# Kernel tuning notes

Hardware: AMD Instinct MI355X
Metric: run time of the kernel (lower is better)

The kernel has to match this reference:

```python
import jax, jax.numpy as jnp
import numpy as np

DIM_IN_Q = 4096
DIM_IN_K = 4096
MSG_DIM = 4096


def setup_inputs() -> dict:
    key = jax.random.key(0)
    ks = jax.random.split(key, 8)
    s_q = 1.0 / np.sqrt(DIM_IN_Q)
    s_l = 1.0 / np.sqrt(MSG_DIM)
    s_k = 1.0 / np.sqrt(DIM_IN_K)
    return {
        # forward args (2-D path; N == msg_dim and M == 6 are structural requirements)
        "data_q": jax.random.normal(ks[0], (MSG_DIM, DIM_IN_Q), jnp.float32),
        "data_k": jax.random.normal(ks[1], (6, DIM_IN_K), jnp.float32),
        # learned parameters (torch nn.Linear layout: [out, in])
        "W_q": jax.random.uniform(ks[2], (MSG_DIM, DIM_IN_Q), jnp.float32, -s_q, s_q),
        "b_q": jax.random.uniform(ks[3], (MSG_DIM,), jnp.float32, -s_q, s_q),
        "W_lin": jax.random.uniform(ks[4], (6, MSG_DIM), jnp.float32, -s_l, s_l),
        "b_lin": jax.random.uniform(ks[5], (6,), jnp.float32, -s_l, s_l),
        "W_k": jax.random.uniform(ks[6], (MSG_DIM, DIM_IN_K), jnp.float32, -s_k, s_k),
        "b_k": jax.random.uniform(ks[7], (MSG_DIM,), jnp.float32, -s_k, s_k),
    }


def _relu6(x):
    return jnp.clip(x, 0.0, 6.0)


def reference(data_q, data_k, W_q, b_q, W_lin, b_lin, W_k, b_k):
    # q: [N=msg_dim, msg_dim]
    q = data_q @ W_q.T + b_q
    # secondary projection over transposed q: [msg_dim, N] -> [msg_dim, 6]
    new_q = q.T @ W_lin.T + b_lin
    # k: [6, msg_dim]
    k = data_k @ W_k.T + b_k
    context = new_q.T  # [6, msg_dim]
    # custom modulation: relu6(k^2 + 2k + context*(1+|k|))
    k_mod = _relu6(jnp.square(k) + 2.0 * k + context * (1.0 + jnp.abs(k)))
    # dot: [msg_dim, 6], scaled by sqrt(msg_dim)
    dot = q @ k_mod.T
    return dot / np.sqrt(MSG_DIM).astype(np.float32)
```

## Files before the change

### kernel.cpp

```cpp
#include <hip/hip_runtime.h>
#include <hip/hip_bf16.h>
#include <stdint.h>

#define NDIM 4096

typedef __attribute__((ext_vector_type(8))) __bf16 bf16x8;
typedef __attribute__((ext_vector_type(4))) float f32x4;

__device__ inline void g2lds16(const void* g, void* l) {
  __builtin_amdgcn_global_load_lds(
      (const __attribute__((address_space(1))) void*)g,
      (__attribute__((address_space(3))) void*)l, 16, 0, 0);
}

__device__ inline unsigned short f2bf(float f) {
  union { float f; uint32_t u; } c; c.f = f;
  uint32_t u = c.u;
  uint32_t r = ((u >> 16) & 1u) + 0x7FFFu;
  return (unsigned short)((u + r) >> 16);
}

__device__ inline float bf2f(ushort u) {
  union { uint32_t u; float f; } c; c.u = ((uint32_t)u) << 16;
  return c.f;
}

__global__ __launch_bounds__(256) void convert_kernel(const float* __restrict__ in,
                                                      ushort* __restrict__ out) {
  int idx = blockIdx.x * 256 + threadIdx.x;
  float4 v = ((const float4*)in)[idx];
  ushort4 o;
  o.x = f2bf(v.x); o.y = f2bf(v.y); o.z = f2bf(v.z); o.w = f2bf(v.w);
  ((ushort4*)out)[idx] = o;
}


__device__ inline bf16x8 ldfrag(const ushort* buf, int row, int kk, int lg) {
  int idx = (row * 64 + kk * 32 + lg * 8) ^ ((row & 7) << 3);
  return *(const bf16x8*)&buf[idx];
}

__global__ __launch_bounds__(512, 2) void gemm_q_kernel(const ushort* __restrict__ Abf,
                                                        const ushort* __restrict__ Bbf,
                                                        const float* __restrict__ bias,
                                                        ushort* __restrict__ qout) {
  __shared__ __align__(16) ushort As[2][16384];
  __shared__ __align__(16) ushort Bs[2][16384];

  const int tid = threadIdx.x;
  const int wg = blockIdx.x;
  const int swz = (wg & 7) * 32 + (wg >> 3);
  const int i0 = (swz >> 4) * 256;
  const int j0 = (swz & 15) * 256;

  const int lane = tid & 63, wid = tid >> 6;
  const int wr = wid >> 2, wc = wid & 3;
  const int l15 = lane & 15, lg = lane >> 4;

  const int srow = tid >> 3;
  const int scol = ((tid & 7) ^ (srow & 7)) * 8;

#define STAGE(tensor, r0, k0v, buf)                                          \
  {                                                                          \
    _Pragma("unroll")                                                        \
    for (int i_ = 0; i_ < 4; ++i_) {                                         \
      g2lds16(tensor + (size_t)((r0) + i_ * 64 + srow) * NDIM + (k0v) + scol,\
              (void*)&buf[i_ * 4096 + tid * 8]);                             \
    }                                                                        \
  }

  f32x4 acc[8][4] = {};

  STAGE(Abf, i0, 0, As[0]);
  STAGE(Bbf, j0, 0, Bs[0]);
  STAGE(Abf, i0, 64, As[1]);
  STAGE(Bbf, j0, 64, Bs[1]);
  asm volatile("s_waitcnt vmcnt(8)" ::: "memory");
  __builtin_amdgcn_sched_barrier(0);
  __builtin_amdgcn_s_barrier();
  __builtin_amdgcn_sched_barrier(0);

  for (int kt = 0; kt < 64; ++kt) {
    const int cur = kt & 1;
    const ushort* A = As[cur];
    const ushort* B = Bs[cur];

    bf16x8 a0[4][2], a1[4][2], bfr[4][2];
#pragma unroll
    for (int m = 0; m < 4; ++m)
#pragma unroll
      for (int kk = 0; kk < 2; ++kk)
        a0[m][kk] = ldfrag(A, wr * 128 + m * 16 + l15, kk, lg);
#pragma unroll
    for (int n = 0; n < 4; ++n)
#pragma unroll
      for (int kk = 0; kk < 2; ++kk)
        bfr[n][kk] = ldfrag(B, wc * 64 + n * 16 + l15, kk, lg);
#pragma unroll
    for (int m = 0; m < 4; ++m)
#pragma unroll
      for (int kk = 0; kk < 2; ++kk)
        a1[m][kk] = ldfrag(A, wr * 128 + 64 + m * 16 + l15, kk, lg);

    __builtin_amdgcn_s_setprio(1);
#pragma unroll
    for (int kk = 0; kk < 2; ++kk)
#pragma unroll
      for (int m = 0; m < 4; ++m)
#pragma unroll
        for (int n = 0; n < 4; ++n)
          acc[m][n] = __builtin_amdgcn_mfma_f32_16x16x32_bf16(a0[m][kk], bfr[n][kk], acc[m][n], 0, 0, 0);
    __builtin_amdgcn_s_setprio(0);

    asm volatile("s_waitcnt lgkmcnt(0)" ::: "memory");
    __builtin_amdgcn_sched_barrier(0);
    __builtin_amdgcn_s_barrier();
    __builtin_amdgcn_sched_barrier(0);

    const int knext = ((kt + 2) & 63) * 64;
    STAGE(Abf, i0, knext, As[cur]);
    STAGE(Bbf, j0, knext, Bs[cur]);

    __builtin_amdgcn_s_setprio(1);
#pragma unroll
    for (int kk = 0; kk < 2; ++kk)
#pragma unroll
      for (int m = 0; m < 4; ++m)
#pragma unroll
        for (int n = 0; n < 4; ++n)
          acc[m + 4][n] = __builtin_amdgcn_mfma_f32_16x16x32_bf16(a1[m][kk], bfr[n][kk], acc[m + 4][n], 0, 0, 0);
    __builtin_amdgcn_s_setprio(0);

    asm volatile("s_waitcnt vmcnt(8)" ::: "memory");
    __builtin_amdgcn_sched_barrier(0);
    __builtin_amdgcn_s_barrier();
    __builtin_amdgcn_sched_barrier(0);
  }

  float bv[4];
#pragma unroll
  for (int n = 0; n < 4; ++n) bv[n] = bias[j0 + wc * 64 + n * 16 + l15];
#pragma unroll
  for (int m = 0; m < 8; ++m) {
    const int row = i0 + wr * 128 + m * 16 + lg * 4;
#pragma unroll
    for (int n = 0; n < 4; ++n) {
      const int col = j0 + wc * 64 + n * 16 + l15;
#pragma unroll
      for (int r = 0; r < 4; ++r)
        qout[(size_t)(row + r) * NDIM + col] = f2bf(acc[m][n][r] + bv[n]);
    }
  }
#undef STAGE
}

__global__ __launch_bounds__(256) void gemv_k_kernel(const float* __restrict__ data_k,
                                                     const float* __restrict__ W_k,
                                                     const float* __restrict__ b_k,
                                                     float* __restrict__ k_out) {
  const int wave = threadIdx.x >> 6, lane = threadIdx.x & 63;
  const int m = blockIdx.x * 4 + wave;
  const float4* W = (const float4*)(W_k + (size_t)m * NDIM);
  const float4* D = (const float4*)data_k;
  float acc[6] = {0.f, 0.f, 0.f, 0.f, 0.f, 0.f};
  for (int it = lane; it < NDIM / 4; it += 64) {
    float4 w = W[it];
#pragma unroll
    for (int j = 0; j < 6; ++j) {
      float4 d = D[j * (NDIM / 4) + it];
      acc[j] += w.x * d.x + w.y * d.y + w.z * d.z + w.w * d.w;
    }
  }
#pragma unroll
  for (int j = 0; j < 6; ++j)
#pragma unroll
    for (int off = 1; off < 64; off <<= 1) acc[j] += __shfl_xor(acc[j], off);
  if (lane == 0) {
    const float bv = b_k[m];
#pragma unroll
    for (int j = 0; j < 6; ++j) k_out[j * NDIM + m] = acc[j] + bv;
  }
}

__global__ __launch_bounds__(256) void newq_kernel(const ushort* __restrict__ q,
                                                   const float* __restrict__ W_lin,
                                                   float* __restrict__ newq_t) {
  const int m = blockIdx.x * 256 + threadIdx.x;
  const int n0 = blockIdx.y * 128;
  float acc[6] = {0.f, 0.f, 0.f, 0.f, 0.f, 0.f};
  for (int n = n0; n < n0 + 128; ++n) {
    const float qv = bf2f(q[(size_t)n * NDIM + m]);
#pragma unroll
    for (int j = 0; j < 6; ++j) acc[j] += qv * W_lin[j * NDIM + n];
  }
#pragma unroll
  for (int j = 0; j < 6; ++j) atomicAdd(&newq_t[j * NDIM + m], acc[j]);
}

__global__ __launch_bounds__(256) void kmod_kernel(const float* __restrict__ k_in,
                                                   const float* __restrict__ newq_t,
                                                   const float* __restrict__ b_lin,
                                                   float* __restrict__ k_mod) {
  const int idx = blockIdx.x * 256 + threadIdx.x;
  const int j = idx >> 12;
  const float kv = k_in[idx];
  const float ctx = newq_t[idx] + b_lin[j];
  float v = kv * kv + 2.f * kv + ctx * (1.f + fabsf(kv));
  v = fminf(fmaxf(v, 0.f), 6.f);
  k_mod[idx] = v;
}

__global__ __launch_bounds__(256) void dot_kernel(const ushort* __restrict__ q,
                                                  const float* __restrict__ k_mod,
                                                  float* __restrict__ out) {
  const int wave = threadIdx.x >> 6, lane = threadIdx.x & 63;
  const int n = blockIdx.x * 4 + wave;
  const uint4* Q = (const uint4*)(q + (size_t)n * NDIM);
  float acc[6] = {0.f, 0.f, 0.f, 0.f, 0.f, 0.f};
  for (int it = lane; it < 512; it += 64) {
    uint4 v = Q[it];
    float qf[8];
    qf[0] = __builtin_bit_cast(float, v.x << 16);
    qf[1] = __builtin_bit_cast(float, v.x & 0xffff0000u);
    qf[2] = __builtin_bit_cast(float, v.y << 16);
    qf[3] = __builtin_bit_cast(float, v.y & 0xffff0000u);
    qf[4] = __builtin_bit_cast(float, v.z << 16);
    qf[5] = __builtin_bit_cast(float, v.z & 0xffff0000u);
    qf[6] = __builtin_bit_cast(float, v.w << 16);
    qf[7] = __builtin_bit_cast(float, v.w & 0xffff0000u);
#pragma unroll
    for (int j = 0; j < 6; ++j) {
      const float4* KM = (const float4*)(k_mod + j * NDIM);
      float4 k0 = KM[it * 2], k1 = KM[it * 2 + 1];
      acc[j] += qf[0] * k0.x + qf[1] * k0.y + qf[2] * k0.z + qf[3] * k0.w
              + qf[4] * k1.x + qf[5] * k1.y + qf[6] * k1.z + qf[7] * k1.w;
    }
  }
#pragma unroll
  for (int j = 0; j < 6; ++j)
#pragma unroll
    for (int off = 1; off < 64; off <<= 1) acc[j] += __shfl_xor(acc[j], off);
  if (lane == 0) {
#pragma unroll
    for (int j = 0; j < 6; ++j) out[n * 6 + j] = acc[j] * 0.015625f;
  }
}

extern "C" void kernel_launch(void* const* d_in, const int* in_sizes, int n_in,
                              void* d_out, int out_size, void* d_ws, size_t ws_size,
                              hipStream_t stream) {
  const float* data_q = (const float*)d_in[0];
  const float* data_k = (const float*)d_in[1];
  const float* W_q    = (const float*)d_in[2];
  const float* b_q    = (const float*)d_in[3];
  const float* W_lin  = (const float*)d_in[4];
  const float* b_lin  = (const float*)d_in[5];
  const float* W_k    = (const float*)d_in[6];
  const float* b_k    = (const float*)d_in[7];
  float* out = (float*)d_out;

  char* ws = (char*)d_ws;
  ushort* Abf   = (ushort*)ws;
  ushort* Bbf   = (ushort*)(ws + ((size_t)32 << 20));
  ushort* q_bf  = (ushort*)(ws + ((size_t)64 << 20));
  float*  k_arr = (float*)(ws + ((size_t)96 << 20));
  float*  newq  = k_arr + 6 * NDIM;
  float*  kmod  = newq + 6 * NDIM;

  hipMemsetAsync(newq, 0, 6 * NDIM * sizeof(float), stream);

  convert_kernel<<<16384, 256, 0, stream>>>(data_q, Abf);
  convert_kernel<<<16384, 256, 0, stream>>>(W_q, Bbf);
  gemm_q_kernel<<<256, 512, 0, stream>>>(Abf, Bbf, b_q, q_bf);
  gemv_k_kernel<<<1024, 256, 0, stream>>>(data_k, W_k, b_k, k_arr);
  newq_kernel<<<dim3(16, 32), 256, 0, stream>>>(q_bf, W_lin, newq);
  kmod_kernel<<<96, 256, 0, stream>>>(k_arr, newq, b_lin, kmod);
  dot_kernel<<<1024, 256, 0, stream>>>(q_bf, kmod, out);
}
```

Baseline: 450.6 us.

## Restructure GEMM main loop into four half-tile phases and merge conversion launches

Splits the 256x256 block tile's LDS buffers into 128-row halves and rewrites the K loop as four phases. Each phase loads one A or B half-fragment from LDS, issues the global-to-LDS prefetch of one half of the next K tile, and runs a quarter of the MFMAs, with barriers in between (an 8-wave ping-pong style schedule). The aim is to interleave memory traffic with matrix math more finely, at the cost of more barriers per iteration and a changed per-wave row mapping. Separately, the two fp32-to-bf16 conversion kernels are merged into one launch to save launch overhead.

```diff
diff --git a/kernel.cpp b/kernel.cpp
--- a/kernel.cpp
+++ b/kernel.cpp
@@ -25,9 +25,14 @@
   return c.f;
 }
 
-__global__ __launch_bounds__(256) void convert_kernel(const float* __restrict__ in,
-                                                      ushort* __restrict__ out) {
-  int idx = blockIdx.x * 256 + threadIdx.x;
+__global__ __launch_bounds__(256) void convert2_kernel(const float* __restrict__ a,
+                                                       ushort* __restrict__ oa,
+                                                       const float* __restrict__ b,
+                                                       ushort* __restrict__ ob) {
+  const int bid = blockIdx.x;
+  const float* in = (bid < 16384) ? a : b;
+  ushort* out = (bid < 16384) ? oa : ob;
+  const int idx = (bid & 16383) * 256 + threadIdx.x;
   float4 v = ((const float4*)in)[idx];
   ushort4 o;
   o.x = f2bf(v.x); o.y = f2bf(v.y); o.z = f2bf(v.z); o.w = f2bf(v.w);
@@ -35,17 +40,17 @@
 }
 
 
-__device__ inline bf16x8 ldfrag(const ushort* buf, int row, int kk, int lg) {
-  int idx = (row * 64 + kk * 32 + lg * 8) ^ ((row & 7) << 3);
-  return *(const bf16x8*)&buf[idx];
+__device__ inline bf16x8 ldfrag(const ushort* half_buf, int rrow, int blk) {
+  int idx = (rrow * 64 + blk * 8) ^ ((rrow & 7) << 3);
+  return *(const bf16x8*)&half_buf[idx];
 }
 
 __global__ __launch_bounds__(512, 2) void gemm_q_kernel(const ushort* __restrict__ Abf,
                                                         const ushort* __restrict__ Bbf,
                                                         const float* __restrict__ bias,
                                                         ushort* __restrict__ qout) {
-  __shared__ __align__(16) ushort As[2][16384];
-  __shared__ __align__(16) ushort Bs[2][16384];
+  __shared__ __align__(16) ushort As[2][2][8192];
+  __shared__ __align__(16) ushort Bs[2][2][8192];
 
   const int tid = threadIdx.x;
   const int wg = blockIdx.x;
@@ -60,81 +65,79 @@
   const int srow = tid >> 3;
   const int scol = ((tid & 7) ^ (srow & 7)) * 8;
 
-#define STAGE(tensor, r0, k0v, buf)                                          \
-  {                                                                          \
-    _Pragma("unroll")                                                        \
-    for (int i_ = 0; i_ < 4; ++i_) {                                         \
-      g2lds16(tensor + (size_t)((r0) + i_ * 64 + srow) * NDIM + (k0v) + scol,\
-              (void*)&buf[i_ * 4096 + tid * 8]);                             \
-    }                                                                        \
-  }
+#define STAGE_HALF(tensor, grow0, k0v, dst)                                    \
+  {                                                                            \
+    g2lds16((tensor) + (size_t)((grow0) + srow) * NDIM + (k0v) + scol,         \
+            (void*)&(dst)[tid * 8]);                                           \
+    g2lds16((tensor) + (size_t)((grow0) + 64 + srow) * NDIM + (k0v) + scol,    \
+            (void*)&(dst)[4096 + tid * 8]);                                    \
+  }
+
+#define SB __builtin_amdgcn_sched_barrier(0)
+#define BAR { SB; __builtin_amdgcn_s_barrier(); SB; }
+#define LGKM0 { asm volatile("s_waitcnt lgkmcnt(0)" ::: "memory"); SB; }
 
   f32x4 acc[8][4] = {};
-
-  STAGE(Abf, i0, 0, As[0]);
-  STAGE(Bbf, j0, 0, Bs[0]);
-  STAGE(Abf, i0, 64, As[1]);
-  STAGE(Bbf, j0, 64, Bs[1]);
-  asm volatile("s_waitcnt vmcnt(8)" ::: "memory");
-  __builtin_amdgcn_sched_barrier(0);
-  __builtin_amdgcn_s_barrier();
-  __builtin_amdgcn_sched_barrier(0);
+  bf16x8 a[4][2];
+  bf16x8 b[2][2][2];
+
+#define DSR_A(bufc, mh)                                                        \
+  _Pragma("unroll") for (int mi = 0; mi < 4; ++mi)                             \
+  _Pragma("unroll") for (int kk = 0; kk < 2; ++kk)                             \
+    a[mi][kk] = ldfrag(As[bufc][mh], wr * 64 + mi * 16 + l15, kk * 4 + lg);
+
+#define DSR_B(bufc, nh)                                                        \
+  _Pragma("unroll") for (int ni = 0; ni < 2; ++ni)                             \
+  _Pragma("unroll") for (int kk = 0; kk < 2; ++kk)                             \
+    b[nh][ni][kk] = ldfrag(Bs[bufc][wc >> 1],                                  \
+                           (wc & 1) * 64 + ((nh) * 2 + ni) * 16 + l15,         \
+                           kk * 4 + lg);
+
+#define MFMA_PH(mh, nh)                                                        \
+  __builtin_amdgcn_s_setprio(1);                                              \
+  _Pragma("unroll") for (int kk = 0; kk < 2; ++kk)                             \
+  _Pragma("unroll") for (int mi = 0; mi < 4; ++mi)                             \
+  _Pragma("unroll") for (int ni = 0; ni < 2; ++ni)                             \
+    acc[(mh) * 4 + mi][(nh) * 2 + ni] = __builtin_amdgcn_mfma_f32_16x16x32_bf16( \
+        a[mi][kk], b[nh][ni][kk], acc[(mh) * 4 + mi][(nh) * 2 + ni], 0, 0, 0); \
+  __builtin_amdgcn_s_setprio(0);
+
+  STAGE_HALF(Abf, i0 + 0,   0, As[0][0]);
+  STAGE_HALF(Bbf, j0 + 0,   0, Bs[0][0]);
+  STAGE_HALF(Bbf, j0 + 128, 0, Bs[0][1]);
+  STAGE_HALF(Abf, i0 + 128, 0, As[0][1]);
+  asm volatile("s_waitcnt vmcnt(2)" ::: "memory");
+  BAR;
 
   for (int kt = 0; kt < 64; ++kt) {
-    const int cur = kt & 1;
-    const ushort* A = As[cur];
-    const ushort* B = Bs[cur];
-
-    bf16x8 a0[4][2], a1[4][2], bfr[4][2];
-#pragma unroll
-    for (int m = 0; m < 4; ++m)
-#pragma unroll
-      for (int kk = 0; kk < 2; ++kk)
-        a0[m][kk] = ldfrag(A, wr * 128 + m * 16 + l15, kk, lg);
-#pragma unroll
-    for (int n = 0; n < 4; ++n)
-#pragma unroll
-      for (int kk = 0; kk < 2; ++kk)
-        bfr[n][kk] = ldfrag(B, wc * 64 + n * 16 + l15, kk, lg);
-#pragma unroll
-    for (int m = 0; m < 4; ++m)
-#pragma unroll
-      for (int kk = 0; kk < 2; ++kk)
-        a1[m][kk] = ldfrag(A, wr * 128 + 64 + m * 16 + l15, kk, lg);
-
-    __builtin_amdgcn_s_setprio(1);
-#pragma unroll
-    for (int kk = 0; kk < 2; ++kk)
-#pragma unroll
-      for (int m = 0; m < 4; ++m)
-#pragma unroll
-        for (int n = 0; n < 4; ++n)
-          acc[m][n] = __builtin_amdgcn_mfma_f32_16x16x32_bf16(a0[m][kk], bfr[n][kk], acc[m][n], 0, 0, 0);
-    __builtin_amdgcn_s_setprio(0);
-
-    asm volatile("s_waitcnt lgkmcnt(0)" ::: "memory");
-    __builtin_amdgcn_sched_barrier(0);
-    __builtin_amdgcn_s_barrier();
-    __builtin_amdgcn_sched_barrier(0);
-
-    const int knext = ((kt + 2) & 63) * 64;
-    STAGE(Abf, i0, knext, As[cur]);
-    STAGE(Bbf, j0, knext, Bs[cur]);
-
-    __builtin_amdgcn_s_setprio(1);
-#pragma unroll
-    for (int kk = 0; kk < 2; ++kk)
-#pragma unroll
-      for (int m = 0; m < 4; ++m)
-#pragma unroll
-        for (int n = 0; n < 4; ++n)
-          acc[m + 4][n] = __builtin_amdgcn_mfma_f32_16x16x32_bf16(a1[m][kk], bfr[n][kk], acc[m + 4][n], 0, 0, 0);
-    __builtin_amdgcn_s_setprio(0);
-
-    asm volatile("s_waitcnt vmcnt(8)" ::: "memory");
-    __builtin_amdgcn_sched_barrier(0);
-    __builtin_amdgcn_s_barrier();
-    __builtin_amdgcn_sched_barrier(0);
+    const int bufc = kt & 1, bufn = bufc ^ 1;
+    const int kn1 = ((kt + 1) & 63) * 64;
+
+    DSR_A(bufc, 0);
+    DSR_B(bufc, 0);
+    STAGE_HALF(Abf, i0 + 0, kn1, As[bufn][0]);
+    BAR; LGKM0;
+    MFMA_PH(0, 0);
+    BAR;
+
+    DSR_B(bufc, 1);
+    STAGE_HALF(Bbf, j0 + 0, kn1, Bs[bufn][0]);
+    BAR; LGKM0;
+    MFMA_PH(0, 1);
+    asm volatile("s_waitcnt vmcnt(4)" ::: "memory");
+    BAR;
+
+    DSR_A(bufc, 1);
+    STAGE_HALF(Bbf, j0 + 128, kn1, Bs[bufn][1]);
+    BAR; LGKM0;
+    MFMA_PH(1, 0);
+    BAR;
+
+    STAGE_HALF(Abf, i0 + 128, kn1, As[bufn][1]);
+    BAR;
+    MFMA_PH(1, 1);
+    asm volatile("s_waitcnt vmcnt(2)" ::: "memory");
+    BAR;
   }
 
   float bv[4];
@@ -142,7 +145,7 @@
   for (int n = 0; n < 4; ++n) bv[n] = bias[j0 + wc * 64 + n * 16 + l15];
 #pragma unroll
   for (int m = 0; m < 8; ++m) {
-    const int row = i0 + wr * 128 + m * 16 + lg * 4;
+    const int row = i0 + (m >> 2) * 128 + wr * 64 + (m & 3) * 16 + lg * 4;
 #pragma unroll
     for (int n = 0; n < 4; ++n) {
       const int col = j0 + wc * 64 + n * 16 + l15;
@@ -151,7 +154,13 @@
         qout[(size_t)(row + r) * NDIM + col] = f2bf(acc[m][n][r] + bv[n]);
     }
   }
-#undef STAGE
+#undef STAGE_HALF
+#undef DSR_A
+#undef DSR_B
+#undef MFMA_PH
+#undef BAR
+#undef LGKM0
+#undef SB
 }
 
 __global__ __launch_bounds__(256) void gemv_k_kernel(const float* __restrict__ data_k,
@@ -269,8 +278,7 @@
 
   hipMemsetAsync(newq, 0, 6 * NDIM * sizeof(float), stream);
 
-  convert_kernel<<<16384, 256, 0, stream>>>(data_q, Abf);
-  convert_kernel<<<16384, 256, 0, stream>>>(W_q, Bbf);
+  convert2_kernel<<<32768, 256, 0, stream>>>(data_q, Abf, W_q, Bbf);
   gemm_q_kernel<<<256, 512, 0, stream>>>(Abf, Bbf, b_q, q_bf);
   gemv_k_kernel<<<1024, 256, 0, stream>>>(data_k, W_k, b_k, k_arr);
   newq_kernel<<<dim3(16, 32), 256, 0, stream>>>(q_bf, W_lin, newq);
```

New measurement: 360.5 us. 1.25x faster.
